# Kernel optimization log

Hardware: AMD Instinct MI355X
Metric: run time of the kernel (lower is better)

## Reference

```python
import jax, jax.numpy as jnp
import numpy as np

B, T, NIN, H = 256, 100, 64, 1024


def _lstm_cell(x, h, c, Wih, Whh, bih, bhh):
    # torch.nn.LSTMCell: gates = x@Wih^T + bih + h@Whh^T + bhh, order (i, f, g, o)
    gates = x @ Wih.T + bih + h @ Whh.T + bhh  # [B, 4H]
    i, f, g, o = jnp.split(gates, 4, axis=-1)
    i = jax.nn.sigmoid(i)
    f = jax.nn.sigmoid(f)
    g = jnp.tanh(g)
    o = jax.nn.sigmoid(o)
    c_new = f * c + i * g
    h_new = o * jnp.tanh(c_new)
    return h_new, c_new


def setup_inputs() -> dict:
    key = jax.random.key(0)
    ks = jax.random.split(key, 17)
    s_in = 1.0 / np.sqrt(H)
    d = {"x": jax.random.normal(ks[0], (B, T, NIN), dtype=jnp.float32)}
    dims_in = [NIN, H, H, H]
    ki = 1
    for layer in range(1, 5):
        din = dims_in[layer - 1]
        d[f"Wih{layer}"] = jax.random.normal(ks[ki], (4 * H, din), dtype=jnp.float32) * s_in; ki += 1
        d[f"Whh{layer}"] = jax.random.normal(ks[ki], (4 * H, H), dtype=jnp.float32) * s_in; ki += 1
        d[f"bih{layer}"] = jax.random.normal(ks[ki], (4 * H,), dtype=jnp.float32) * s_in; ki += 1
        d[f"bhh{layer}"] = jax.random.normal(ks[ki], (4 * H,), dtype=jnp.float32) * s_in; ki += 1
        ks = jax.random.split(ks[-1], 17)
        ki = 0
    return d


def reference(x, Wih1, Whh1, bih1, bhh1, Wih2, Whh2, bih2, bhh2,
              Wih3, Whh3, bih3, bhh3, Wih4, Whh4, bih4, bhh4):
    batch = x.shape[0]
    params = ((Wih1, Whh1, bih1, bhh1), (Wih2, Whh2, bih2, bhh2),
              (Wih3, Whh3, bih3, bhh3), (Wih4, Whh4, bih4, bhh4))
    zeros = jnp.zeros((batch, H), dtype=x.dtype)
    init = tuple((zeros, zeros) for _ in range(4))

    def step(carry, xt):
        new_carry = []
        inp = xt
        for (h, c), (Wih, Whh, bih, bhh) in zip(carry, params):
            h, c = _lstm_cell(inp, h, c, Wih, Whh, bih, bhh)
            new_carry.append((h, c))
            inp = h
        return tuple(new_carry), inp  # top-layer h

    xs = jnp.swapaxes(x, 0, 1)  # [T, B, NIN]
    carry, hs = jax.lax.scan(step, init, xs)
    out = jnp.swapaxes(hs, 0, 1)  # [B, T, H]
    c4 = carry[3][1]
    return out, c4
```

## Files before the change

kernel.cpp:

```cpp
#include <hip/hip_runtime.h>
#include <hip/hip_bf16.h>

typedef __hip_bfloat16 bf16;
typedef unsigned short u16;
typedef unsigned int u32;
typedef __attribute__((ext_vector_type(8))) short bf16x8;
typedef __attribute__((ext_vector_type(4))) float f32x4;

#define BATCH 256
#define TLEN 100
#define HDIM 1024
#define G4 4096
#define OUT_HT (BATCH * TLEN * HDIM)

#define WS_WP 0u
#define WS_BIAS 59244544u
#define WS_XT 59310080u
#define WS_H 62586880u
#define WS_FLAGS (WS_H + 4194304u)

__device__ __forceinline__ float sigm(float x) { return 1.0f / (1.0f + __expf(-x)); }
__device__ __forceinline__ float tanh_(float x) { return 2.0f / (1.0f + __expf(-2.0f * x)) - 1.0f; }

__device__ __forceinline__ void gl_lds16(const void* g, void* l) {
  __builtin_amdgcn_global_load_lds((const __attribute__((address_space(1))) u32*)g,
                                   (__attribute__((address_space(3))) u32*)l, 16, 0, 0);
}


__global__ void pack_w(const float* __restrict__ wih, const float* __restrict__ whh,
                       bf16* __restrict__ dst, int NC, int din) {
  int i = blockIdx.x * 256 + threadIdx.x;
  if (i >= 32 * NC * 128 * 64) return;
  int k6 = i & 63;
  int r = (i >> 6) & 127;
  int jc = i >> 13;
  int c = jc % NC;
  int j = jc / NC;
  int grow = ((r >> 5) << 10) + j * 32 + (r & 31);
  int k = c * 64 + k6;
  float v = (k < din) ? wih[grow * din + k] : whh[(grow << 10) + (k - din)];
  dst[(jc << 13) + (r << 6) + (k6 ^ ((r & 7) << 3))] = __float2bfloat16(v);
}

__global__ void pack_bias(const float* __restrict__ a, const float* __restrict__ b,
                          float* __restrict__ dst) {
  int i = blockIdx.x * 256 + threadIdx.x;
  if (i < G4) dst[i] = a[i] + b[i];
}

__global__ void pack_x(const float* __restrict__ x, bf16* __restrict__ xT) {
  int i = blockIdx.x * 256 + threadIdx.x;
  if (i >= TLEN * BATCH * 64) return;
  int k = i & 63;
  int b = (i >> 6) & 255;
  int t = i >> 14;
  xT[(t << 14) + (b << 6) + (k ^ ((b & 7) << 3))] = __float2bfloat16(x[(b * TLEN + t) * 64 + k]);
}


__global__ void __launch_bounds__(512, 2)
lstm_main(const u16* __restrict__ Wp, const float* __restrict__ biasc,
          const u16* __restrict__ xT, u16* __restrict__ hbuf,
          float* __restrict__ out, u32* __restrict__ flags) {
  __shared__ __align__(16) u16 smem[73728];

  const int tid = threadIdx.x;
  const int lane = tid & 63;
  const int wave = tid >> 6;
  const int wg = blockIdx.x;
  const int layer = wg >> 6;
  const int sub = wg & 63;
  const int bt = sub >> 5;
  const int b0 = bt * 128;
  const int h0 = (sub & 31) * 32;

  const int NC = (layer == 0) ? 17 : 32;
  const int T0 = (layer == 0) ? 1 : 16;
  const u16* Wsl = Wp + ((layer == 0) ? 0u : (4456448u + (u32)(layer - 1) * 8388608u))
                 + (u32)(sub & 31) * (u32)NC * 8192u;

  const int nn = tid & 31;
  float bias_r[4];
#pragma unroll
  for (int g = 0; g < 4; ++g) bias_r[g] = biasc[layer * G4 + g * HDIM + h0 + nn];

  const int r0 = (tid >> 5) * 8;
  float cst[8];
#pragma unroll
  for (int k = 0; k < 8; ++k) cst[k] = 0.0f;

  const int opu0 = (wave * 2) * 512 + lane * 8;
  const int opu1 = opu0 + 512;

  const int mh = (wave >> 2) & 1;
  const int nh = (wave >> 1) & 1;
  const int kh = wave & 1;
  const int lrow = lane & 15;
  const int lswz = (lane & 7) << 4;
  const int kbyte = kh * 64 + ((lane >> 4) << 4);
  const int kx = kbyte ^ lswz;

  float* G0 = (float*)smem;
  float* G1 = (float*)((char*)smem + 67584);

  u32* myflag = flags + (layer * 2 + bt) * 32 + (sub & 31);
  const u32 jj = lane & 31;
  const u32* pPrev = flags + (((layer > 0 ? layer - 1 : 0) * 2 + bt) * 32) + jj;
  const u32* pNext = flags + (((layer < 3 ? layer + 1 : 3) * 2 + bt) * 32) + jj;
  const u32* pOwn  = flags + ((layer * 2 + bt) * 32) + jj;

  for (int t = 0; t < TLEN; ++t) {
    if (wave == 0) {
      const bool needP = (layer > 0) && (lane < 32);
      const bool needN = (layer < 3) && (lane < 32) && (t >= 2);
      const bool needO = (lane >= 32) && (t >= 1);
      while (true) {
        bool ok = true;
        if (needP) ok &= (__hip_atomic_load(pPrev, __ATOMIC_RELAXED, __HIP_MEMORY_SCOPE_AGENT) >= (u32)(t + 1));
        if (needN) ok &= (__hip_atomic_load(pNext, __ATOMIC_RELAXED, __HIP_MEMORY_SCOPE_AGENT) >= (u32)(t - 1));
        if (needO) ok &= (__hip_atomic_load(pOwn,  __ATOMIC_RELAXED, __HIP_MEMORY_SCOPE_AGENT) >= (u32)t);
        if (__all(ok)) break;
        __builtin_amdgcn_s_sleep(1);
      }
      __builtin_amdgcn_fence(__ATOMIC_ACQUIRE, "agent");
    }
    __syncthreads();

    const u16* aBase0 = ((layer == 0) ? (xT + (u32)t * 16384u)
                                      : (hbuf + (u32)((layer - 1) * 2 + (t & 1)) * 262144u))
                      + b0 * 64;
    const u16* aBase1 = hbuf + (u32)(layer * 2 + ((t + 1) & 1)) * 262144u + b0 * 64;

    f32x4 acc[4][4];
#pragma unroll
    for (int mt = 0; mt < 4; ++mt)
#pragma unroll
      for (int nt = 0; nt < 4; ++nt) acc[mt][nt] = (f32x4)(0.0f);

    auto issueA = [&](int c, int slot) {
      const u16* src = (c < T0) ? (aBase0 + c * 16384) : (aBase1 + (c - T0) * 16384);
      gl_lds16(src + opu0, smem + slot * 8192 + (wave * 2) * 512);
      gl_lds16(src + opu1, smem + slot * 8192 + (wave * 2 + 1) * 512);
    };
    auto issueB = [&](int c, int slot) {
      const u16* src = Wsl + c * 8192;
      gl_lds16(src + opu0, smem + 32768 + slot * 8192 + (wave * 2) * 512);
      gl_lds16(src + opu1, smem + 32768 + slot * 8192 + (wave * 2 + 1) * 512);
    };

    issueB(0, 0);
    issueA(0, 0);
    issueB(1, 1);
    issueA(1, 1);
    issueB(2, 2);

    for (int c = 0; c < NC; ++c) {
      {
        int ca = c + 2; int cca = (ca < NC) ? ca : (NC - 1);
        issueA(cca, ca & 3);
        int cb = c + 3; int ccb = (cb < NC) ? cb : (NC - 1);
        issueB(ccb, cb % 5);
      }
      asm volatile("s_waitcnt vmcnt(10)" ::: "memory");
      __builtin_amdgcn_s_barrier();

      const char* Abuf = (const char*)smem + (c & 3) * 16384;
      const char* Bbuf = (const char*)smem + 65536 + (c % 5) * 16384;
      bf16x8 a[4], b[4];
#pragma unroll
      for (int mt = 0; mt < 4; ++mt) {
        int row = mh * 64 + mt * 16 + lrow;
        a[mt] = *(const bf16x8*)(Abuf + row * 128 + kx);
      }
#pragma unroll
      for (int nt = 0; nt < 4; ++nt) {
        int row = nh * 64 + nt * 16 + lrow;
        b[nt] = *(const bf16x8*)(Bbuf + row * 128 + kx);
      }
#pragma unroll
      for (int mt = 0; mt < 4; ++mt)
#pragma unroll
        for (int nt = 0; nt < 4; ++nt)
          acc[mt][nt] = __builtin_amdgcn_mfma_f32_16x16x32_bf16(a[mt], b[nt], acc[mt][nt], 0, 0, 0);
    }

    asm volatile("s_waitcnt vmcnt(0)" ::: "memory");
    __syncthreads();

    float* Gw = kh ? G1 : G0;
#pragma unroll
    for (int mt = 0; mt < 4; ++mt)
#pragma unroll
      for (int nt = 0; nt < 4; ++nt) {
        int row = mh * 64 + mt * 16 + (lane >> 4) * 4;
        int col = nh * 64 + nt * 16 + (lane & 15);
#pragma unroll
        for (int r = 0; r < 4; ++r) Gw[(row + r) * 132 + col] = acc[mt][nt][r];
      }
    __syncthreads();

    u16* outSlot = hbuf + (u32)(layer * 2 + (t & 1)) * 262144u;
    const int hcol = h0 + nn;
    const int j2 = hcol >> 6;
    const int colin = hcol & 63;
#pragma unroll
    for (int k = 0; k < 8; ++k) {
      int r = r0 + k;
      float gi = G0[r * 132 + nn]      + G1[r * 132 + nn]      + bias_r[0];
      float gf = G0[r * 132 + 32 + nn] + G1[r * 132 + 32 + nn] + bias_r[1];
      float gg = G0[r * 132 + 64 + nn] + G1[r * 132 + 64 + nn] + bias_r[2];
      float go = G0[r * 132 + 96 + nn] + G1[r * 132 + 96 + nn] + bias_r[3];
      float iv = sigm(gi), fv = sigm(gf), gv = tanh_(gg), ov = sigm(go);
      float cv = fv * cst[k] + iv * gv;
      cst[k] = cv;
      float hv = ov * tanh_(cv);
      int b = b0 + r;
      bf16 hb = __float2bfloat16(hv);
      outSlot[j2 * 16384 + b * 64 + (colin ^ ((b & 7) << 3))] = *(u16*)&hb;
      if (layer == 3) {
        out[((size_t)b * TLEN + t) * HDIM + hcol] = hv;
        if (t == TLEN - 1) out[OUT_HT + (size_t)b * HDIM + hcol] = cv;
      }
    }

    __syncthreads();
    if (tid == 0)
      __hip_atomic_store(myflag, (u32)(t + 1), __ATOMIC_RELEASE, __HIP_MEMORY_SCOPE_AGENT);
  }
}


extern "C" void kernel_launch(void* const* d_in, const int* in_sizes, int n_in,
                              void* d_out, int out_size, void* d_ws, size_t ws_size,
                              hipStream_t stream) {
  const float* x = (const float*)d_in[0];
  const float* Wih[4] = {(const float*)d_in[1], (const float*)d_in[5],
                         (const float*)d_in[9], (const float*)d_in[13]};
  const float* Whh[4] = {(const float*)d_in[2], (const float*)d_in[6],
                         (const float*)d_in[10], (const float*)d_in[14]};
  const float* bih[4] = {(const float*)d_in[3], (const float*)d_in[7],
                         (const float*)d_in[11], (const float*)d_in[15]};
  const float* bhh[4] = {(const float*)d_in[4], (const float*)d_in[8],
                         (const float*)d_in[12], (const float*)d_in[16]};

  char* ws = (char*)d_ws;
  bf16* Wp = (bf16*)(ws + WS_WP);
  float* biasc = (float*)(ws + WS_BIAS);
  bf16* xT = (bf16*)(ws + WS_XT);
  u16* hbuf = (u16*)(ws + WS_H);
  u32* flags = (u32*)(ws + WS_FLAGS);
  float* out = (float*)d_out;

  for (int l = 0; l < 4; ++l) {
    int NC = (l == 0) ? 17 : 32;
    int din = (l == 0) ? 64 : 1024;
    bf16* dst = Wp + ((l == 0) ? 0 : (4456448 + (size_t)(l - 1) * 8388608));
    int total = 32 * NC * 128 * 64;
    pack_w<<<(total + 255) / 256, 256, 0, stream>>>(Wih[l], Whh[l], dst, NC, din);
    pack_bias<<<16, 256, 0, stream>>>(bih[l], bhh[l], biasc + l * 4096);
  }
  pack_x<<<(TLEN * BATCH * 64 + 255) / 256, 256, 0, stream>>>(x, xT);
  hipMemsetAsync(ws + WS_H, 0, 4194304u + 1024u, stream);

  void* args[] = {(void*)&Wp, (void*)&biasc, (void*)&xT, (void*)&hbuf, (void*)&out, (void*)&flags};
  hipLaunchCooperativeKernel((void*)lstm_main, dim3(256), dim3(512), args, 0, stream);
}
```

Before: 3.094 ms.

## Batch input projection over two timesteps to reuse Wih tiles in upper layers

```diff
diff --git a/kernel.cpp b/kernel.cpp
--- a/kernel.cpp
+++ b/kernel.cpp
@@ -75,10 +75,8 @@
   const int b0 = bt * 128;
   const int h0 = (sub & 31) * 32;
 
-  const int NC = (layer == 0) ? 17 : 32;
-  const int T0 = (layer == 0) ? 1 : 16;
   const u16* Wsl = Wp + ((layer == 0) ? 0u : (4456448u + (u32)(layer - 1) * 8388608u))
-                 + (u32)(sub & 31) * (u32)NC * 8192u;
+                 + (u32)(sub & 31) * (u32)((layer == 0) ? 17 : 32) * 8192u;
 
   const int nn = tid & 31;
   float bias_r[4];
@@ -98,8 +96,8 @@
   const int kh = wave & 1;
   const int lrow = lane & 15;
   const int lswz = (lane & 7) << 4;
-  const int kbyte = kh * 64 + ((lane >> 4) << 4);
-  const int kx = kbyte ^ lswz;
+  const int kslot = (lane >> 4) << 4;
+  const int kx2 = (kh * 64 + kslot) ^ lswz;
 
   float* G0 = (float*)smem;
   float* G1 = (float*)((char*)smem + 67584);
@@ -110,27 +108,32 @@
   const u32* pNext = flags + (((layer < 3 ? layer + 1 : 3) * 2 + bt) * 32) + jj;
   const u32* pOwn  = flags + ((layer * 2 + bt) * 32) + jj;
 
-  for (int t = 0; t < TLEN; ++t) {
+  auto waitFlags = [&](int thrP, int thrO, int thrN) {
     if (wave == 0) {
-      const bool needP = (layer > 0) && (lane < 32);
-      const bool needN = (layer < 3) && (lane < 32) && (t >= 2);
-      const bool needO = (lane >= 32) && (t >= 1);
+      const bool needP = (thrP >= 0) && (layer > 0) && (lane < 32);
+      const bool needN = (thrN >= 0) && (layer < 3) && (lane < 32);
+      const bool needO = (thrO >= 0) && (lane >= 32);
       while (true) {
         bool ok = true;
-        if (needP) ok &= (__hip_atomic_load(pPrev, __ATOMIC_RELAXED, __HIP_MEMORY_SCOPE_AGENT) >= (u32)(t + 1));
-        if (needN) ok &= (__hip_atomic_load(pNext, __ATOMIC_RELAXED, __HIP_MEMORY_SCOPE_AGENT) >= (u32)(t - 1));
-        if (needO) ok &= (__hip_atomic_load(pOwn,  __ATOMIC_RELAXED, __HIP_MEMORY_SCOPE_AGENT) >= (u32)t);
+        if (needP) ok &= (__hip_atomic_load(pPrev, __ATOMIC_RELAXED, __HIP_MEMORY_SCOPE_AGENT) >= (u32)thrP);
+        if (needN) ok &= (__hip_atomic_load(pNext, __ATOMIC_RELAXED, __HIP_MEMORY_SCOPE_AGENT) >= (u32)thrN);
+        if (needO) ok &= (__hip_atomic_load(pOwn,  __ATOMIC_RELAXED, __HIP_MEMORY_SCOPE_AGENT) >= (u32)thrO);
         if (__all(ok)) break;
         __builtin_amdgcn_s_sleep(1);
       }
       __builtin_amdgcn_fence(__ATOMIC_ACQUIRE, "agent");
     }
     __syncthreads();
-
-    const u16* aBase0 = ((layer == 0) ? (xT + (u32)t * 16384u)
-                                      : (hbuf + (u32)((layer - 1) * 2 + (t & 1)) * 262144u))
-                      + b0 * 64;
-    const u16* aBase1 = hbuf + (u32)(layer * 2 + ((t + 1) & 1)) * 262144u + b0 * 64;
+  };
+
+  f32x4 accI[4][4];
+
+  auto runStep = [&](int t, bool addI) {
+    const int NC2 = (layer == 0) ? 17 : 16;
+    const int bOff = (layer == 0) ? 0 : 16;
+    const u16* aX = xT + (u32)t * 16384u + b0 * 64;
+    const u16* aH = hbuf + (u32)(layer * 2 + ((t + 1) & 1)) * 262144u + b0 * 64;
+    const int T0 = (layer == 0) ? 1 : 0;
 
     f32x4 acc[4][4];
 #pragma unroll
@@ -139,12 +142,12 @@
       for (int nt = 0; nt < 4; ++nt) acc[mt][nt] = (f32x4)(0.0f);
 
     auto issueA = [&](int c, int slot) {
-      const u16* src = (c < T0) ? (aBase0 + c * 16384) : (aBase1 + (c - T0) * 16384);
+      const u16* src = (c < T0) ? aX : (aH + (u32)(c - T0) * 16384u);
       gl_lds16(src + opu0, smem + slot * 8192 + (wave * 2) * 512);
       gl_lds16(src + opu1, smem + slot * 8192 + (wave * 2 + 1) * 512);
     };
     auto issueB = [&](int c, int slot) {
-      const u16* src = Wsl + c * 8192;
+      const u16* src = Wsl + (u32)(bOff + c) * 8192u;
       gl_lds16(src + opu0, smem + 32768 + slot * 8192 + (wave * 2) * 512);
       gl_lds16(src + opu1, smem + 32768 + slot * 8192 + (wave * 2 + 1) * 512);
     };
@@ -155,11 +158,11 @@
     issueA(1, 1);
     issueB(2, 2);
 
-    for (int c = 0; c < NC; ++c) {
+    for (int c = 0; c < NC2; ++c) {
       {
-        int ca = c + 2; int cca = (ca < NC) ? ca : (NC - 1);
+        int ca = c + 2; int cca = (ca < NC2) ? ca : (NC2 - 1);
         issueA(cca, ca & 3);
-        int cb = c + 3; int ccb = (cb < NC) ? cb : (NC - 1);
+        int cb = c + 3; int ccb = (cb < NC2) ? cb : (NC2 - 1);
         issueB(ccb, cb % 5);
       }
       asm volatile("s_waitcnt vmcnt(10)" ::: "memory");
@@ -169,15 +172,11 @@
       const char* Bbuf = (const char*)smem + 65536 + (c % 5) * 16384;
       bf16x8 a[4], b[4];
 #pragma unroll
-      for (int mt = 0; mt < 4; ++mt) {
-        int row = mh * 64 + mt * 16 + lrow;
-        a[mt] = *(const bf16x8*)(Abuf + row * 128 + kx);
-      }
-#pragma unroll
-      for (int nt = 0; nt < 4; ++nt) {
-        int row = nh * 64 + nt * 16 + lrow;
-        b[nt] = *(const bf16x8*)(Bbuf + row * 128 + kx);
-      }
+      for (int mt = 0; mt < 4; ++mt)
+        a[mt] = *(const bf16x8*)(Abuf + (mh * 64 + mt * 16 + lrow) * 128 + kx2);
+#pragma unroll
+      for (int nt = 0; nt < 4; ++nt)
+        b[nt] = *(const bf16x8*)(Bbuf + (nh * 64 + nt * 16 + lrow) * 128 + kx2);
 #pragma unroll
       for (int mt = 0; mt < 4; ++mt)
 #pragma unroll
@@ -187,6 +186,13 @@
 
     asm volatile("s_waitcnt vmcnt(0)" ::: "memory");
     __syncthreads();
+
+    if (addI) {
+#pragma unroll
+      for (int mt = 0; mt < 4; ++mt)
+#pragma unroll
+        for (int nt = 0; nt < 4; ++nt) acc[mt][nt] += accI[mt][nt];
+    }
 
     float* Gw = kh ? G1 : G0;
 #pragma unroll
@@ -223,10 +229,81 @@
         if (t == TLEN - 1) out[OUT_HT + (size_t)b * HDIM + hcol] = cv;
       }
     }
-
     __syncthreads();
     if (tid == 0)
       __hip_atomic_store(myflag, (u32)(t + 1), __ATOMIC_RELEASE, __HIP_MEMORY_SCOPE_AGENT);
+  };
+
+  for (int tb = 0; tb < TLEN / 2; ++tb) {
+    const int t0 = 2 * tb;
+
+    waitFlags(layer > 0 ? (t0 + 2) : -1,
+              t0 >= 1 ? t0 : -1,
+              t0 >= 1 ? (t0 - 1) : -1);
+
+    if (layer > 0) {
+      const u16* hb0 = hbuf + (u32)((layer - 1) * 2 + (t0 & 1)) * 262144u + b0 * 64;
+      const u16* hb1 = hbuf + (u32)((layer - 1) * 2 + ((t0 + 1) & 1)) * 262144u + b0 * 64;
+
+#pragma unroll
+      for (int mt = 0; mt < 4; ++mt)
+#pragma unroll
+        for (int nt = 0; nt < 4; ++nt) accI[mt][nt] = (f32x4)(0.0f);
+
+      auto issueA1 = [&](int c, int slot) {
+#pragma unroll
+        for (int q = 0; q < 4; ++q) {
+          const u16* base = (q >> 1) ? hb1 : hb0;
+          gl_lds16(base + (u32)c * 16384u + ((wave * 2 + (q & 1)) * 512) + lane * 8,
+                   smem + slot * 16384 + (q >> 1) * 8192 + (wave * 2 + (q & 1)) * 512);
+        }
+      };
+      auto issueB1 = [&](int c, int slot) {
+        const u16* src = Wsl + (u32)c * 8192u;
+        gl_lds16(src + opu0, smem + 49152 + slot * 8192 + (wave * 2) * 512);
+        gl_lds16(src + opu1, smem + 49152 + slot * 8192 + (wave * 2 + 1) * 512);
+      };
+
+      issueA1(0, 0);
+      issueB1(0, 0);
+
+      for (int c = 0; c < 16; ++c) {
+        {
+          int cn = c + 1; int ccn = (cn < 16) ? cn : 15;
+          issueA1(ccn, cn % 3);
+          issueB1(ccn, cn % 3);
+        }
+        asm volatile("s_waitcnt vmcnt(6)" ::: "memory");
+        __builtin_amdgcn_s_barrier();
+
+        const char* Abuf = (const char*)smem + (c % 3) * 32768 + kh * 16384;
+        const char* Bbuf = (const char*)smem + 98304 + (c % 3) * 16384;
+#pragma unroll
+        for (int ks = 0; ks < 2; ++ks) {
+          const int col = (ks * 64 + kslot) ^ lswz;
+          bf16x8 a[4], b[4];
+#pragma unroll
+          for (int mt = 0; mt < 4; ++mt)
+            a[mt] = *(const bf16x8*)(Abuf + (mh * 64 + mt * 16 + lrow) * 128 + col);
+#pragma unroll
+          for (int nt = 0; nt < 4; ++nt)
+            b[nt] = *(const bf16x8*)(Bbuf + (nh * 64 + nt * 16 + lrow) * 128 + col);
+#pragma unroll
+          for (int mt = 0; mt < 4; ++mt)
+#pragma unroll
+            for (int nt = 0; nt < 4; ++nt)
+              accI[mt][nt] = __builtin_amdgcn_mfma_f32_16x16x32_bf16(a[mt], b[nt], accI[mt][nt], 0, 0, 0);
+        }
+      }
+      asm volatile("s_waitcnt vmcnt(0)" ::: "memory");
+      __syncthreads();
+    }
+
+    runStep(t0, (layer > 0) && (kh == 0));
+
+    waitFlags(-1, t0 + 1, -1);
+
+    runStep(t0 + 1, (layer > 0) && (kh == 1));
   }
 }
 
```

Result: slower. 5.445 ms (+76.0%).

## Load MFMA operands directly from global memory instead of LDS-staged pipeline

Applied to the files above, without the earlier changes.

```diff
diff --git a/kernel.cpp b/kernel.cpp
--- a/kernel.cpp
+++ b/kernel.cpp
@@ -21,11 +21,6 @@
 
 __device__ __forceinline__ float sigm(float x) { return 1.0f / (1.0f + __expf(-x)); }
 __device__ __forceinline__ float tanh_(float x) { return 2.0f / (1.0f + __expf(-2.0f * x)) - 1.0f; }
-
-__device__ __forceinline__ void gl_lds16(const void* g, void* l) {
-  __builtin_amdgcn_global_load_lds((const __attribute__((address_space(1))) u32*)g,
-                                   (__attribute__((address_space(3))) u32*)l, 16, 0, 0);
-}
 
 
 __global__ void pack_w(const float* __restrict__ wih, const float* __restrict__ whh,
@@ -63,22 +58,23 @@
 lstm_main(const u16* __restrict__ Wp, const float* __restrict__ biasc,
           const u16* __restrict__ xT, u16* __restrict__ hbuf,
           float* __restrict__ out, u32* __restrict__ flags) {
-  __shared__ __align__(16) u16 smem[73728];
+  __shared__ float G0[128 * 132];
+  __shared__ float G1[128 * 132];
 
   const int tid = threadIdx.x;
   const int lane = tid & 63;
   const int wave = tid >> 6;
   const int wg = blockIdx.x;
-  const int layer = wg >> 6;
-  const int sub = wg & 63;
-  const int bt = sub >> 5;
+  const int layer = (wg & 127) >> 5;
+  const int j = wg & 31;
+  const int bt = wg >> 7;
   const int b0 = bt * 128;
-  const int h0 = (sub & 31) * 32;
+  const int h0 = j * 32;
 
   const int NC = (layer == 0) ? 17 : 32;
-  const int T0 = (layer == 0) ? 1 : 16;
-  const u16* Wsl = Wp + ((layer == 0) ? 0u : (4456448u + (u32)(layer - 1) * 8388608u))
-                 + (u32)(sub & 31) * (u32)NC * 8192u;
+  const char* Wbytes = (const char*)(Wp
+                       + ((layer == 0) ? 0u : (4456448u + (u32)(layer - 1) * 8388608u))
+                       + (u32)j * (u32)NC * 8192u);
 
   const int nn = tid & 31;
   float bias_r[4];
@@ -89,22 +85,24 @@
   float cst[8];
 #pragma unroll
   for (int k = 0; k < 8; ++k) cst[k] = 0.0f;
-
-  const int opu0 = (wave * 2) * 512 + lane * 8;
-  const int opu1 = opu0 + 512;
 
   const int mh = (wave >> 2) & 1;
   const int nh = (wave >> 1) & 1;
   const int kh = wave & 1;
   const int lrow = lane & 15;
   const int lswz = (lane & 7) << 4;
-  const int kbyte = kh * 64 + ((lane >> 4) << 4);
-  const int kx = kbyte ^ lswz;
-
-  float* G0 = (float*)smem;
-  float* G1 = (float*)((char*)smem + 67584);
-
-  u32* myflag = flags + (layer * 2 + bt) * 32 + (sub & 31);
+  const int kslot = (lane >> 4) << 4;
+  const int kx = (kh * 64 + kslot) ^ lswz;
+
+  u32 aOff[4], bOff[4];
+#pragma unroll
+  for (int mt = 0; mt < 4; ++mt)
+    aOff[mt] = (u32)(b0 + mh * 64 + mt * 16 + lrow) * 128u + (u32)kx;
+#pragma unroll
+  for (int nt = 0; nt < 4; ++nt)
+    bOff[nt] = (u32)(nh * 64 + nt * 16 + lrow) * 128u + (u32)kx;
+
+  u32* myflag = flags + (layer * 2 + bt) * 32 + j;
   const u32 jj = lane & 31;
   const u32* pPrev = flags + (((layer > 0 ? layer - 1 : 0) * 2 + bt) * 32) + jj;
   const u32* pNext = flags + (((layer < 3 ? layer + 1 : 3) * 2 + bt) * 32) + jj;
@@ -127,10 +125,10 @@
     }
     __syncthreads();
 
-    const u16* aBase0 = ((layer == 0) ? (xT + (u32)t * 16384u)
-                                      : (hbuf + (u32)((layer - 1) * 2 + (t & 1)) * 262144u))
-                      + b0 * 64;
-    const u16* aBase1 = hbuf + (u32)(layer * 2 + ((t + 1) & 1)) * 262144u + b0 * 64;
+    const char* xb = (const char*)xT + (u32)t * 32768u;
+    const char* hbelow = (const char*)hbuf
+                       + (u32)((layer > 0 ? layer - 1 : 0) * 2 + (t & 1)) * 524288u;
+    const char* hown = (const char*)hbuf + (u32)(layer * 2 + ((t + 1) & 1)) * 524288u;
 
     f32x4 acc[4][4];
 #pragma unroll
@@ -138,55 +136,32 @@
 #pragma unroll
       for (int nt = 0; nt < 4; ++nt) acc[mt][nt] = (f32x4)(0.0f);
 
-    auto issueA = [&](int c, int slot) {
-      const u16* src = (c < T0) ? (aBase0 + c * 16384) : (aBase1 + (c - T0) * 16384);
-      gl_lds16(src + opu0, smem + slot * 8192 + (wave * 2) * 512);
-      gl_lds16(src + opu1, smem + slot * 8192 + (wave * 2 + 1) * 512);
-    };
-    auto issueB = [&](int c, int slot) {
-      const u16* src = Wsl + c * 8192;
-      gl_lds16(src + opu0, smem + 32768 + slot * 8192 + (wave * 2) * 512);
-      gl_lds16(src + opu1, smem + 32768 + slot * 8192 + (wave * 2 + 1) * 512);
-    };
-
-    issueB(0, 0);
-    issueA(0, 0);
-    issueB(1, 1);
-    issueA(1, 1);
-    issueB(2, 2);
-
-    for (int c = 0; c < NC; ++c) {
-      {
-        int ca = c + 2; int cca = (ca < NC) ? ca : (NC - 1);
-        issueA(cca, ca & 3);
-        int cb = c + 3; int ccb = (cb < NC) ? cb : (NC - 1);
-        issueB(ccb, cb % 5);
-      }
-      asm volatile("s_waitcnt vmcnt(10)" ::: "memory");
-      __builtin_amdgcn_s_barrier();
-
-      const char* Abuf = (const char*)smem + (c & 3) * 16384;
-      const char* Bbuf = (const char*)smem + 65536 + (c % 5) * 16384;
+    int cB = 0;
+    auto body = [&](const char* aI) {
+      const char* bI = Wbytes + (u32)cB * 16384u;
+      ++cB;
       bf16x8 a[4], b[4];
 #pragma unroll
-      for (int mt = 0; mt < 4; ++mt) {
-        int row = mh * 64 + mt * 16 + lrow;
-        a[mt] = *(const bf16x8*)(Abuf + row * 128 + kx);
-      }
-#pragma unroll
-      for (int nt = 0; nt < 4; ++nt) {
-        int row = nh * 64 + nt * 16 + lrow;
-        b[nt] = *(const bf16x8*)(Bbuf + row * 128 + kx);
-      }
+      for (int mt = 0; mt < 4; ++mt) a[mt] = *(const bf16x8*)(aI + aOff[mt]);
+#pragma unroll
+      for (int nt = 0; nt < 4; ++nt) b[nt] = *(const bf16x8*)(bI + bOff[nt]);
 #pragma unroll
       for (int mt = 0; mt < 4; ++mt)
 #pragma unroll
         for (int nt = 0; nt < 4; ++nt)
           acc[mt][nt] = __builtin_amdgcn_mfma_f32_16x16x32_bf16(a[mt], b[nt], acc[mt][nt], 0, 0, 0);
+    };
+
+    if (layer == 0) {
+      body(xb);
+#pragma unroll 2
+      for (int c = 0; c < 16; ++c) body(hown + (u32)c * 32768u);
+    } else {
+#pragma unroll 2
+      for (int c = 0; c < 16; ++c) body(hbelow + (u32)c * 32768u);
+#pragma unroll 2
+      for (int c = 0; c < 16; ++c) body(hown + (u32)c * 32768u);
     }
-
-    asm volatile("s_waitcnt vmcnt(0)" ::: "memory");
-    __syncthreads();
 
     float* Gw = kh ? G1 : G0;
 #pragma unroll
```

Measured after the change: 3.933 ms. +27.1%, slower.

## Double K-chunk size for hidden layers and remap workgroups by batch tile

Applied to the files above, without the earlier changes.

```diff
diff --git a/kernel.cpp b/kernel.cpp
--- a/kernel.cpp
+++ b/kernel.cpp
@@ -63,22 +63,21 @@
 lstm_main(const u16* __restrict__ Wp, const float* __restrict__ biasc,
           const u16* __restrict__ xT, u16* __restrict__ hbuf,
           float* __restrict__ out, u32* __restrict__ flags) {
-  __shared__ __align__(16) u16 smem[73728];
+  __shared__ __align__(16) u16 smem[81920];
 
   const int tid = threadIdx.x;
   const int lane = tid & 63;
   const int wave = tid >> 6;
   const int wg = blockIdx.x;
-  const int layer = wg >> 6;
-  const int sub = wg & 63;
-  const int bt = sub >> 5;
+  const int layer = (wg & 127) >> 5;
+  const int j = wg & 31;
+  const int bt = wg >> 7;
   const int b0 = bt * 128;
-  const int h0 = (sub & 31) * 32;
-
-  const int NC = (layer == 0) ? 17 : 32;
-  const int T0 = (layer == 0) ? 1 : 16;
+  const int h0 = j * 32;
+
+  const int NC64 = (layer == 0) ? 17 : 32;
   const u16* Wsl = Wp + ((layer == 0) ? 0u : (4456448u + (u32)(layer - 1) * 8388608u))
-                 + (u32)(sub & 31) * (u32)NC * 8192u;
+                 + (u32)j * (u32)NC64 * 8192u;
 
   const int nn = tid & 31;
   float bias_r[4];
@@ -90,7 +89,7 @@
 #pragma unroll
   for (int k = 0; k < 8; ++k) cst[k] = 0.0f;
 
-  const int opu0 = (wave * 2) * 512 + lane * 8;
+  const int opu0 = wave * 1024 + lane * 8;
   const int opu1 = opu0 + 512;
 
   const int mh = (wave >> 2) & 1;
@@ -98,13 +97,13 @@
   const int kh = wave & 1;
   const int lrow = lane & 15;
   const int lswz = (lane & 7) << 4;
-  const int kbyte = kh * 64 + ((lane >> 4) << 4);
-  const int kx = kbyte ^ lswz;
+  const int kslot = (lane >> 4) << 4;
+  const int kx64 = (kh * 64 + kslot) ^ lswz;
 
   float* G0 = (float*)smem;
   float* G1 = (float*)((char*)smem + 67584);
 
-  u32* myflag = flags + (layer * 2 + bt) * 32 + (sub & 31);
+  u32* myflag = flags + (layer * 2 + bt) * 32 + j;
   const u32 jj = lane & 31;
   const u32* pPrev = flags + (((layer > 0 ? layer - 1 : 0) * 2 + bt) * 32) + jj;
   const u32* pNext = flags + (((layer < 3 ? layer + 1 : 3) * 2 + bt) * 32) + jj;
@@ -127,62 +126,116 @@
     }
     __syncthreads();
 
-    const u16* aBase0 = ((layer == 0) ? (xT + (u32)t * 16384u)
-                                      : (hbuf + (u32)((layer - 1) * 2 + (t & 1)) * 262144u))
-                      + b0 * 64;
-    const u16* aBase1 = hbuf + (u32)(layer * 2 + ((t + 1) & 1)) * 262144u + b0 * 64;
-
     f32x4 acc[4][4];
 #pragma unroll
     for (int mt = 0; mt < 4; ++mt)
 #pragma unroll
       for (int nt = 0; nt < 4; ++nt) acc[mt][nt] = (f32x4)(0.0f);
 
-    auto issueA = [&](int c, int slot) {
-      const u16* src = (c < T0) ? (aBase0 + c * 16384) : (aBase1 + (c - T0) * 16384);
-      gl_lds16(src + opu0, smem + slot * 8192 + (wave * 2) * 512);
-      gl_lds16(src + opu1, smem + slot * 8192 + (wave * 2 + 1) * 512);
-    };
-    auto issueB = [&](int c, int slot) {
-      const u16* src = Wsl + c * 8192;
-      gl_lds16(src + opu0, smem + 32768 + slot * 8192 + (wave * 2) * 512);
-      gl_lds16(src + opu1, smem + 32768 + slot * 8192 + (wave * 2 + 1) * 512);
-    };
-
-    issueB(0, 0);
-    issueA(0, 0);
-    issueB(1, 1);
-    issueA(1, 1);
-    issueB(2, 2);
-
-    for (int c = 0; c < NC; ++c) {
-      {
-        int ca = c + 2; int cca = (ca < NC) ? ca : (NC - 1);
-        issueA(cca, ca & 3);
-        int cb = c + 3; int ccb = (cb < NC) ? cb : (NC - 1);
-        issueB(ccb, cb % 5);
-      }
-      asm volatile("s_waitcnt vmcnt(10)" ::: "memory");
-      __builtin_amdgcn_s_barrier();
-
-      const char* Abuf = (const char*)smem + (c & 3) * 16384;
-      const char* Bbuf = (const char*)smem + 65536 + (c % 5) * 16384;
-      bf16x8 a[4], b[4];
-#pragma unroll
-      for (int mt = 0; mt < 4; ++mt) {
-        int row = mh * 64 + mt * 16 + lrow;
-        a[mt] = *(const bf16x8*)(Abuf + row * 128 + kx);
-      }
-#pragma unroll
-      for (int nt = 0; nt < 4; ++nt) {
-        int row = nh * 64 + nt * 16 + lrow;
-        b[nt] = *(const bf16x8*)(Bbuf + row * 128 + kx);
-      }
-#pragma unroll
-      for (int mt = 0; mt < 4; ++mt)
+    if (layer == 0) {
+      const u16* aBase0 = xT + (u32)t * 16384u + b0 * 64;
+      const u16* aBase1 = hbuf + (u32)(0 * 2 + ((t + 1) & 1)) * 262144u + b0 * 64;
+
+      auto issueA = [&](int c, int slot) {
+        const u16* src = (c < 1) ? aBase0 : (aBase1 + (u32)(c - 1) * 16384u);
+        gl_lds16(src + opu0, smem + slot * 8192 + wave * 1024);
+        gl_lds16(src + opu1, smem + slot * 8192 + wave * 1024 + 512);
+      };
+      auto issueB = [&](int c, int slot) {
+        const u16* src = Wsl + (u32)c * 8192u;
+        gl_lds16(src + opu0, smem + 32768 + slot * 8192 + wave * 1024);
+        gl_lds16(src + opu1, smem + 32768 + slot * 8192 + wave * 1024 + 512);
+      };
+
+      issueB(0, 0);
+      issueA(0, 0);
+      issueB(1, 1);
+      issueA(1, 1);
+      issueB(2, 2);
+
+      for (int c = 0; c < 17; ++c) {
+        {
+          int ca = c + 2; int cca = (ca < 17) ? ca : 16;
+          issueA(cca, ca & 3);
+          int cb = c + 3; int ccb = (cb < 17) ? cb : 16;
+          issueB(ccb, cb % 5);
+        }
+        asm volatile("s_waitcnt vmcnt(10)" ::: "memory");
+        __builtin_amdgcn_s_barrier();
+
+        const char* Abuf = (const char*)smem + (c & 3) * 16384;
+        const char* Bbuf = (const char*)smem + 65536 + (c % 5) * 16384;
+        bf16x8 a[4], b[4];
+#pragma unroll
+        for (int mt = 0; mt < 4; ++mt)
+          a[mt] = *(const bf16x8*)(Abuf + (mh * 64 + mt * 16 + lrow) * 128 + kx64);
 #pragma unroll
         for (int nt = 0; nt < 4; ++nt)
-          acc[mt][nt] = __builtin_amdgcn_mfma_f32_16x16x32_bf16(a[mt], b[nt], acc[mt][nt], 0, 0, 0);
+          b[nt] = *(const bf16x8*)(Bbuf + (nh * 64 + nt * 16 + lrow) * 128 + kx64);
+#pragma unroll
+        for (int mt = 0; mt < 4; ++mt)
+#pragma unroll
+          for (int nt = 0; nt < 4; ++nt)
+            acc[mt][nt] = __builtin_amdgcn_mfma_f32_16x16x32_bf16(a[mt], b[nt], acc[mt][nt], 0, 0, 0);
+      }
+    } else {
+      const u16* hin   = hbuf + (u32)((layer - 1) * 2 + (t & 1)) * 262144u + b0 * 64;
+      const u16* hprev = hbuf + (u32)(layer * 2 + ((t + 1) & 1)) * 262144u + b0 * 64;
+
+      auto issueA = [&](int c, int slot) {
+#pragma unroll
+        for (int s = 0; s < 2; ++s) {
+          int ci = 2 * c + s;
+          const u16* img = (ci < 16) ? (hin + (u32)ci * 16384u)
+                                     : (hprev + (u32)(ci - 16) * 16384u);
+          gl_lds16(img + opu0, smem + slot * 16384 + s * 8192 + wave * 1024);
+          gl_lds16(img + opu1, smem + slot * 16384 + s * 8192 + wave * 1024 + 512);
+        }
+      };
+      auto issueB = [&](int c, int slot) {
+        const u16* src = Wsl + (u32)c * 16384u;
+#pragma unroll
+        for (int q = 0; q < 4; ++q)
+          gl_lds16(src + wave * 2048 + q * 512 + lane * 8,
+                   smem + 32768 + slot * 16384 + wave * 2048 + q * 512);
+      };
+
+      issueA(0, 0);
+      issueB(0, 0);
+      issueB(1, 1);
+
+      for (int c = 0; c < 16; ++c) {
+        asm volatile("s_waitcnt vmcnt(4)" ::: "memory");
+        __builtin_amdgcn_s_barrier();
+
+        const char* Abuf = (const char*)smem + (c & 1) * 32768 + kh * 16384;
+        const char* Bbuf = (const char*)smem + 65536 + (c % 3) * 32768 + kh * 16384;
+        bf16x8 a[2][4], b[2][4];
+#pragma unroll
+        for (int ks = 0; ks < 2; ++ks) {
+          const int col = (ks * 64 + kslot) ^ lswz;
+#pragma unroll
+          for (int mt = 0; mt < 4; ++mt)
+            a[ks][mt] = *(const bf16x8*)(Abuf + (mh * 64 + mt * 16 + lrow) * 128 + col);
+#pragma unroll
+          for (int nt = 0; nt < 4; ++nt)
+            b[ks][nt] = *(const bf16x8*)(Bbuf + (nh * 64 + nt * 16 + lrow) * 128 + col);
+        }
+        asm volatile("s_waitcnt lgkmcnt(0)" ::: "memory");
+        {
+          int ca = c + 1; int cca = (ca < 16) ? ca : 15;
+          issueA(cca, ca & 1);
+          int cb = c + 2; int ccb = (cb < 16) ? cb : 15;
+          issueB(ccb, cb % 3);
+        }
+#pragma unroll
+        for (int ks = 0; ks < 2; ++ks)
+#pragma unroll
+          for (int mt = 0; mt < 4; ++mt)
+#pragma unroll
+            for (int nt = 0; nt < 4; ++nt)
+              acc[mt][nt] = __builtin_amdgcn_mfma_f32_16x16x32_bf16(a[ks][mt], b[ks][nt], acc[mt][nt], 0, 0, 0);
+      }
     }
 
     asm volatile("s_waitcnt vmcnt(0)" ::: "memory");
```

Result: slower. 3.382 ms (+9.3%).
